# Kernel optimization log

Measured on AMD Instinct MI355X. Metric: run time of the kernel, lower is better.

## Reference

```python
import jax, jax.numpy as jnp
import numpy as np

N = 86016      # 1024 graphs x 84 nodes
E = 4194304    # directed edges
H = 32         # hidden size
B = 1024       # graphs per batch
NPG = 84       # nodes per graph (hardcoded in original forward)
DEPTH = 4      # args.depth
NEG_SLOPE = 0.2


def setup_inputs() -> dict:
    key = jax.random.key(0)
    ks = jax.random.split(key, 12)
    s = 0.1
    return {
        "x": jax.random.normal(ks[0], (N, 1), jnp.float32),
        "edge_index": jax.random.randint(ks[1], (2, E), 0, N, jnp.int64 if jax.config.jax_enable_x64 else jnp.int32),
        "edge_attr": jax.random.normal(ks[2], (E, 2), jnp.float32),
        "W0": jax.random.normal(ks[3], (1, H), jnp.float32) * s,
        "Ws": jax.random.normal(ks[4], (DEPTH - 1, H, H), jnp.float32) * s,
        "att_src": jax.random.normal(ks[5], (DEPTH, H), jnp.float32) * s,
        "att_dst": jax.random.normal(ks[6], (DEPTH, H), jnp.float32) * s,
        "We": jax.random.normal(ks[7], (DEPTH, 2, H), jnp.float32) * s,
        "att_edge": jax.random.normal(ks[8], (DEPTH, H), jnp.float32) * s,
        "bias": jnp.zeros((DEPTH, H), jnp.float32),
        "lin_w": jax.random.normal(ks[9], (H, 1), jnp.float32) * s,
        "lin_b": jnp.zeros((1,), jnp.float32),
    }


def _gat_layer(h_in, src, dst, ea, W, a_s, a_d, We_l, a_e, b):
    """PyG GATConv, heads=1, edge_dim set, self-loops already appended.
    src/dst: [E+N] indices; ea: [E+N, edge_dim] edge attrs (with mean-filled loops)."""
    h = h_in @ W                                  # [N, H]
    alpha_src = h @ a_s                           # [N]
    alpha_dst = h @ a_d                           # [N]
    # fold lin_edge + att_edge: (ea @ We) @ a_e == ea @ (We @ a_e) -> avoids [E,H]
    alpha_edge = ea @ (We_l @ a_e)                # [E+N]
    logits = alpha_src[src] + alpha_dst[dst] + alpha_edge
    logits = jnp.where(logits >= 0, logits, NEG_SLOPE * logits)  # leaky_relu(0.2)
    # segment softmax over destination nodes (every node has a self-loop -> nonempty)
    m = jax.ops.segment_max(logits, dst, num_segments=N)
    w = jnp.exp(logits - m[dst])
    denom = jax.ops.segment_sum(w, dst, num_segments=N)
    alpha = w / denom[dst]                        # [E+N]
    out = jax.ops.segment_sum(alpha[:, None] * h[src], dst, num_segments=N)
    return out + b


def reference(x, edge_index, edge_attr, W0, Ws, att_src, att_dst, We, att_edge, bias, lin_w, lin_b):
    src0, dst0 = edge_index[0], edge_index[1]
    # add_self_loops with fill_value='mean': per-dst mean of incoming edge attrs
    deg = jax.ops.segment_sum(jnp.ones((E,), x.dtype), dst0, num_segments=N)
    ea_loop = jax.ops.segment_sum(edge_attr, dst0, num_segments=N) / jnp.maximum(deg, 1.0)[:, None]
    loops = jnp.arange(N, dtype=src0.dtype)
    src = jnp.concatenate([src0, loops])
    dst = jnp.concatenate([dst0, loops])
    ea = jnp.concatenate([edge_attr, ea_loop], axis=0)

    # layer 0 (+ relu; dropout is identity in eval)
    h = _gat_layer(x, src, dst, ea, W0, att_src[0], att_dst[0], We[0], att_edge[0], bias[0])
    h = jax.nn.relu(h)
    # middle layers
    for i in range(1, DEPTH - 1):
        h = _gat_layer(h, src, dst, ea, Ws[i - 1], att_src[i], att_dst[i], We[i], att_edge[i], bias[i])
        h = jax.nn.relu(h)
    # last layer: no relu/dropout
    h = _gat_layer(h, src, dst, ea, Ws[DEPTH - 2], att_src[DEPTH - 1], att_dst[DEPTH - 1],
                   We[DEPTH - 1], att_edge[DEPTH - 1], bias[DEPTH - 1])

    # global_add_pool over 84-node graphs, then linear + relu
    graph_ids = jnp.repeat(jnp.arange(B), NPG)    # [N]
    pooled = jax.ops.segment_sum(h, graph_ids, num_segments=B)  # [B, H]
    return jax.nn.relu(pooled @ lin_w + lin_b)    # [B, 1]
```

## Files before the change

### kernel.cpp

```cpp
#include <hip/hip_runtime.h>

#define N_NODES 86016
#define N_EDGES 4194304
#define HID 32
#define B_GR 1024
#define NPG 84
#define NEG 0.2f

#define NCH 512
#define CHE 8192
#define NB  512
#define NPB 168
#define SRCMASK 0x1FFFF

typedef float floatx2 __attribute__((ext_vector_type(2)));

constexpr size_t O_REC   = 0;
constexpr size_t O_CM    = O_REC  + (size_t)N_EDGES * 8;
constexpr size_t O_HT    = O_CM   + (size_t)NB * NCH * 4;
constexpr size_t O_HB    = O_HT   + (size_t)N_NODES * HID;
constexpr size_t O_AS    = O_HB   + (size_t)N_NODES * HID * 4;
constexpr size_t O_AD    = O_AS   + (size_t)N_NODES * 4;
constexpr size_t O_ROW   = O_AD   + (size_t)N_NODES * 4;
constexpr size_t O_BTOT  = O_ROW  + (size_t)(N_NODES + 1) * 4 + 12;
constexpr size_t O_BBASE = O_BTOT + (size_t)NB * 4;
constexpr size_t O_FOLD  = O_BBASE + (size_t)(NB + 1) * 4 + 12;

__device__ __forceinline__ unsigned short f2bf(float f) {
    unsigned u = __float_as_uint(f);
    u += 0x7FFFu + ((u >> 16) & 1u);
    return (unsigned short)(u >> 16);
}

__global__ __launch_bounds__(1024) void k_hist(const int* __restrict__ dst, int* __restrict__ cm) {
    __shared__ int cnt[NB];
    int t = threadIdx.x, c = blockIdx.x;
    if (t < NB) cnt[t] = 0;
    __syncthreads();
    int base = c * CHE;
#pragma unroll
    for (int k = 0; k < 8; ++k) {
        int d = dst[base + k * 1024 + t];
        atomicAdd(&cnt[(unsigned)d / NPB], 1);
    }
    __syncthreads();
    if (t < NB) cm[t * NCH + c] = cnt[t];
}

__global__ __launch_bounds__(512) void k_scanchunks(int* __restrict__ cm, int* __restrict__ btot) {
    __shared__ int sa[NCH], sb[NCH];
    int b = blockIdx.x, t = threadIdx.x;
    sa[t] = cm[b * NCH + t];
    __syncthreads();
    int* s = sa; int* d = sb;
    for (int off = 1; off < NCH; off <<= 1) {
        d[t] = s[t] + (t >= off ? s[t - off] : 0);
        __syncthreads();
        int* tmp = s; s = d; d = tmp;
    }
    cm[b * NCH + t] = t ? s[t - 1] : 0;
    if (t == 0) btot[b] = s[NCH - 1];
}

__global__ void k_scanbuckets(const int* __restrict__ btot, int* __restrict__ bbase,
                              int* __restrict__ row,
                              const float* __restrict__ We, const float* __restrict__ ae,
                              float* __restrict__ fold) {
    __shared__ int sa[NB], sb[NB];
    int t = threadIdx.x;
    if (t < 8) {
        int l = t >> 1, c = t & 1;
        float s = 0.f;
        for (int j = 0; j < 32; ++j) s += We[l * 64 + c * 32 + j] * ae[l * 32 + j];
        fold[t] = s;
    }
    sa[t] = btot[t];
    __syncthreads();
    int* s = sa; int* d = sb;
    for (int off = 1; off < NB; off <<= 1) {
        d[t] = s[t] + (t >= off ? s[t - off] : 0);
        __syncthreads();
        int* tmp = s; s = d; d = tmp;
    }
    bbase[t] = t ? s[t - 1] : 0;
    if (t == NB - 1) { bbase[NB] = s[NB - 1]; row[N_NODES] = s[NB - 1]; }
}

__global__ __launch_bounds__(1024) void k_place(const int* __restrict__ ei,
                                                const float2* __restrict__ ea,
                                                const int* __restrict__ cm,
                                                const int* __restrict__ bbase,
                                                int2* __restrict__ rec) {
    __shared__ int cnt[NB];
    __shared__ int base[NB];
    int t = threadIdx.x, c = blockIdx.x;
    if (t < NB) cnt[t] = 0;
    __syncthreads();
    int eb = c * CHE;
    int wd0[8], bin[8], rnk[8];
    unsigned pk[8];
#pragma unroll
    for (int k = 0; k < 8; ++k) {
        int e = eb + k * 1024 + t;
        int s = ei[e];
        int d = ei[N_EDGES + e];
        float2 a = ea[e];
        int b = (unsigned)d / NPB;
        int dn = d - b * NPB;
        wd0[k] = s | (dn << 17);
        pk[k] = ((unsigned)f2bf(a.y) << 16) | f2bf(a.x);
        bin[k] = b;
        rnk[k] = atomicAdd(&cnt[b], 1);
    }
    __syncthreads();
    if (t < NB) base[t] = bbase[t] + cm[t * NCH + c];
    __syncthreads();
#pragma unroll
    for (int k = 0; k < 8; ++k)
        rec[base[bin[k]] + rnk[k]] = make_int2(wd0[k], (int)pk[k]);
}

__global__ __launch_bounds__(1024) void k_sort(int2* __restrict__ rec,
                                               const int* __restrict__ bbase,
                                               int* __restrict__ row) {
    __shared__ int cnt[256], tmp[256], ebase[256];
    int b = blockIdx.x, t = threadIdx.x;
    int n0 = b * NPB;
    int beg = bbase[b], end = bbase[b + 1], m = end - beg;
    if (t < 256) cnt[t] = 0;
    __syncthreads();
    int2 rv[12];
    int dr[12];
    int cv = 0;
    for (int i = t; i < m; i += 1024) {
        int2 r = rec[beg + i];
        int dn = ((unsigned)r.x >> 17) & 0xFF;
        int rnk = atomicAdd(&cnt[dn], 1);
        if (cv < 12) { rv[cv] = r; dr[cv] = dn | (rnk << 8); }
        cv++;
    }
    __syncthreads();
    int* s = cnt; int* d = tmp;
    for (int off = 1; off < 256; off <<= 1) {
        int v = 0;
        if (t < 256) v = s[t] + (t >= off ? s[t - off] : 0);
        __syncthreads();
        if (t < 256) d[t] = v;
        __syncthreads();
        int* tp = s; s = d; d = tp;
    }
    if (t < 256) ebase[t] = t ? s[t - 1] : 0;
    __syncthreads();
    if (t < NPB) row[n0 + t] = beg + ebase[t];
    int ncv = cv < 12 ? cv : 12;
    for (int k = 0; k < ncv; ++k) {
        int dn = dr[k] & 0xFF;
        int rnk = dr[k] >> 8;
        rec[beg + ebase[dn] + rnk] = rv[k];
    }
}

__device__ __forceinline__ void store_fp8_pair(unsigned short* __restrict__ hout,
                                               int n, int j, float acc) {
    float p = __shfl_xor(acc, 1);
    if (!(j & 1)) {
        int pk = __builtin_amdgcn_cvt_pk_fp8_f32(acc, p, 0, false);
        hout[(n << 4) + (j >> 1)] = (unsigned short)pk;
    }
}

__global__ void k_transform0(const float* __restrict__ x, const float* __restrict__ W0,
                             const float* __restrict__ as_w, const float* __restrict__ ad_w,
                             unsigned short* __restrict__ hout, float* __restrict__ as_arr,
                             float* __restrict__ ad_arr) {
    int tid = blockIdx.x * 256 + threadIdx.x;
    int j = tid & 31;
    int n = tid >> 5;
    float acc = x[n] * W0[j];
    store_fp8_pair(hout, n, j, acc);
    float v1 = acc * as_w[j], v2 = acc * ad_w[j];
#pragma unroll
    for (int m = 16; m >= 1; m >>= 1) {
        v1 += __shfl_xor(v1, m);
        v2 += __shfl_xor(v2, m);
    }
    if (j == 0) { as_arr[n] = v1; ad_arr[n] = v2; }
}

__global__ void k_transform(const float* __restrict__ hin, const float* __restrict__ W,
                            const float* __restrict__ as_w, const float* __restrict__ ad_w,
                            unsigned short* __restrict__ hout, float* __restrict__ as_arr,
                            float* __restrict__ ad_arr) {
    __shared__ float Wl[1024];
    int t = threadIdx.x;
#pragma unroll
    for (int i = 0; i < 4; ++i) Wl[t + i * 256] = W[t + i * 256];
    __syncthreads();
    int tid = blockIdx.x * 256 + t;
    int j = tid & 31;
    int n = tid >> 5;
    float hv = hin[tid];
    float acc = 0.f;
#pragma unroll
    for (int k = 0; k < 32; ++k) acc += __shfl(hv, k, 32) * Wl[k * 32 + j];
    store_fp8_pair(hout, n, j, acc);
    float v1 = acc * as_w[j], v2 = acc * ad_w[j];
#pragma unroll
    for (int m = 16; m >= 1; m >>= 1) {
        v1 += __shfl_xor(v1, m);
        v2 += __shfl_xor(v2, m);
    }
    if (j == 0) { as_arr[n] = v1; ad_arr[n] = v2; }
}

__device__ __forceinline__ void acc4_fp8(float w, int word, float* acc) {
    floatx2 v01 = __builtin_amdgcn_cvt_pk_f32_fp8(word, false);
    floatx2 v23 = __builtin_amdgcn_cvt_pk_f32_fp8(word, true);
    acc[0] = fmaf(w, v01.x, acc[0]);
    acc[1] = fmaf(w, v01.y, acc[1]);
    acc[2] = fmaf(w, v23.x, acc[2]);
    acc[3] = fmaf(w, v23.y, acc[3]);
}

__device__ __forceinline__ void edge_body(int2 r, const int2* __restrict__ hv,
                                          const float* __restrict__ as_arr,
                                          float c_dst, float f0, float f1, int dl,
                                          float* acc, float& den, float& esum) {
    int s = r.x & SRCMASK;
    int2 h = hv[(s << 2) + dl];
    float a = as_arr[s];
    float ax = __uint_as_float((unsigned)r.y << 16);
    float ay = __uint_as_float((unsigned)r.y & 0xFFFF0000u);
    float ed = fmaf(ax, f0, ay * f1);
    float lg = a + c_dst + ed;
    lg = fmaxf(lg, NEG * lg);
    float w = __expf(lg);
    den += w;
    esum += ed;
    acc4_fp8(w, h.x, acc);
    acc4_fp8(w, h.y, acc + 4);
}

__global__ void k_gather(const unsigned short* __restrict__ hT, const int2* __restrict__ rec,
                         const int* __restrict__ row,
                         const float* __restrict__ as_arr, const float* __restrict__ ad_arr,
                         const float* __restrict__ fold, const float* __restrict__ bias,
                         float* __restrict__ out, int do_relu) {
    const int2* hv = (const int2*)hT;
    int lane = threadIdx.x & 63;
    int n = blockIdx.x * 4 + (threadIdx.x >> 6);
    int slot = lane >> 2;
    int dl = lane & 3;
    int beg = row[n], end = row[n + 1];
    float c_dst = ad_arr[n];
    float f0 = fold[0], f1 = fold[1];
    float acc[8] = {0.f, 0.f, 0.f, 0.f, 0.f, 0.f, 0.f, 0.f};
    float den = 0.f, esum = 0.f;
    int e = beg;
    for (; e + 32 <= end; e += 32) {
        int2 r0 = rec[e + slot];
        int2 r1 = rec[e + 16 + slot];
        edge_body(r0, hv, as_arr, c_dst, f0, f1, dl, acc, den, esum);
        edge_body(r1, hv, as_arr, c_dst, f0, f1, dl, acc, den, esum);
    }
    for (; e + 16 <= end; e += 16) {
        int2 r = rec[e + slot];
        edge_body(r, hv, as_arr, c_dst, f0, f1, dl, acc, den, esum);
    }
    {
        int ee = e + slot;
        if (ee < end)
            edge_body(rec[ee], hv, as_arr, c_dst, f0, f1, dl, acc, den, esum);
    }
#pragma unroll
    for (int m = 4; m <= 32; m <<= 1) {
#pragma unroll
        for (int k = 0; k < 8; ++k) acc[k] += __shfl_xor(acc[k], m);
        den += __shfl_xor(den, m);
        esum += __shfl_xor(esum, m);
    }
    int dg = end - beg;
    float el = esum / fmaxf((float)dg, 1.0f);
    float lg = as_arr[n] + c_dst + el;
    lg = fmaxf(lg, NEG * lg);
    float w = __expf(lg);
    den += w;
    int2 hs = hv[(n << 2) + dl];
    acc4_fp8(w, hs.x, acc);
    acc4_fp8(w, hs.y, acc + 4);
    float rden = 1.0f / den;
    float o[8];
#pragma unroll
    for (int k = 0; k < 8; ++k) {
        o[k] = acc[k] * rden + bias[8 * dl + k];
        if (do_relu) o[k] = fmaxf(o[k], 0.f);
    }
    if (slot == 0) {
        float4 v0 = {o[0], o[1], o[2], o[3]};
        float4 v1 = {o[4], o[5], o[6], o[7]};
        *(float4*)(out + (n << 5) + 8 * dl) = v0;
        *(float4*)(out + (n << 5) + 8 * dl + 4) = v1;
    }
}

__global__ void k_pool(const float* __restrict__ h, const float* __restrict__ lw,
                       const float* __restrict__ lb, float* __restrict__ out) {
    int lane = threadIdx.x & 63;
    int g = blockIdx.x * 4 + (threadIdx.x >> 6);
    int j = lane & 31;
    int half = lane >> 5;
    const float* base = h + (size_t)g * NPG * HID;
    float acc = 0.f;
    for (int i = half; i < NPG; i += 2) acc += base[i * HID + j];
    acc += __shfl_xor(acc, 32);
    float v = acc * lw[j];
#pragma unroll
    for (int m = 16; m >= 1; m >>= 1) v += __shfl_xor(v, m);
    if (lane == 0) out[g] = fmaxf(v + lb[0], 0.f);
}

extern "C" void kernel_launch(void* const* d_in, const int* in_sizes, int n_in,
                              void* d_out, int out_size, void* d_ws, size_t ws_size,
                              hipStream_t stream) {
    const float* x        = (const float*)d_in[0];
    const int*   ei       = (const int*)d_in[1];
    const float* eattr    = (const float*)d_in[2];
    const float* W0       = (const float*)d_in[3];
    const float* Ws       = (const float*)d_in[4];
    const float* att_src  = (const float*)d_in[5];
    const float* att_dst  = (const float*)d_in[6];
    const float* We       = (const float*)d_in[7];
    const float* att_edge = (const float*)d_in[8];
    const float* bias     = (const float*)d_in[9];
    const float* lin_w    = (const float*)d_in[10];
    const float* lin_b    = (const float*)d_in[11];
    float* out = (float*)d_out;

    char* w = (char*)d_ws;
    int2*           rec    = (int2*)(w + O_REC);
    int*            cm     = (int*)(w + O_CM);
    unsigned short* hT     = (unsigned short*)(w + O_HT);
    float*          hB     = (float*)(w + O_HB);
    float*          as_arr = (float*)(w + O_AS);
    float*          ad_arr = (float*)(w + O_AD);
    int*            row    = (int*)(w + O_ROW);
    int*            btot   = (int*)(w + O_BTOT);
    int*            bbase  = (int*)(w + O_BBASE);
    float*          fold   = (float*)(w + O_FOLD);

    k_hist<<<NCH, 1024, 0, stream>>>(ei + N_EDGES, cm);
    k_scanchunks<<<NB, 512, 0, stream>>>(cm, btot);
    k_scanbuckets<<<1, NB, 0, stream>>>(btot, bbase, row, We, att_edge, fold);
    k_place<<<NCH, 1024, 0, stream>>>(ei, (const float2*)eattr, cm, bbase, rec);
    k_sort<<<NB, 1024, 0, stream>>>(rec, bbase, row);

    k_transform0<<<N_NODES * HID / 256, 256, 0, stream>>>(x, W0, att_src, att_dst,
                                                          hT, as_arr, ad_arr);
    k_gather<<<N_NODES / 4, 256, 0, stream>>>(hT, rec, row, as_arr, ad_arr,
                                              fold, bias, hB, 1);
    for (int l = 1; l < 4; ++l) {
        k_transform<<<N_NODES * HID / 256, 256, 0, stream>>>(
            hB, Ws + (size_t)(l - 1) * HID * HID, att_src + l * HID, att_dst + l * HID,
            hT, as_arr, ad_arr);
        k_gather<<<N_NODES / 4, 256, 0, stream>>>(hT, rec, row, as_arr, ad_arr,
                                                  fold + 2 * l, bias + l * HID, hB,
                                                  (l < 3) ? 1 : 0);
    }

    k_pool<<<B_GR / 4, 256, 0, stream>>>(hB, lin_w, lin_b, out);
}
```

Before: 518.9 us.

## Compute edge weights once per lane and broadcast via shuffles in gather

The gather kernel now assigns one edge per lane for logit/exp computation over 64-edge chunks, then broadcasts source index and weight to feature lanes with shuffles, removing the 4x redundant record loads, attention loads and exponentials. Accumulation switches to packed two-wide FMA on float2 accumulators. The cost is extra shuffles and wasted work on inactive lanes in partial chunks, which is significant since average degree is below 64.

```diff
diff --git a/kernel.cpp b/kernel.cpp
--- a/kernel.cpp
+++ b/kernel.cpp
@@ -213,32 +213,11 @@
     if (j == 0) { as_arr[n] = v1; ad_arr[n] = v2; }
 }
 
-__device__ __forceinline__ void acc4_fp8(float w, int word, float* acc) {
+__device__ __forceinline__ void acc4_fp8_pk(floatx2 w2, int word, floatx2* acc) {
     floatx2 v01 = __builtin_amdgcn_cvt_pk_f32_fp8(word, false);
     floatx2 v23 = __builtin_amdgcn_cvt_pk_f32_fp8(word, true);
-    acc[0] = fmaf(w, v01.x, acc[0]);
-    acc[1] = fmaf(w, v01.y, acc[1]);
-    acc[2] = fmaf(w, v23.x, acc[2]);
-    acc[3] = fmaf(w, v23.y, acc[3]);
-}
-
-__device__ __forceinline__ void edge_body(int2 r, const int2* __restrict__ hv,
-                                          const float* __restrict__ as_arr,
-                                          float c_dst, float f0, float f1, int dl,
-                                          float* acc, float& den, float& esum) {
-    int s = r.x & SRCMASK;
-    int2 h = hv[(s << 2) + dl];
-    float a = as_arr[s];
-    float ax = __uint_as_float((unsigned)r.y << 16);
-    float ay = __uint_as_float((unsigned)r.y & 0xFFFF0000u);
-    float ed = fmaf(ax, f0, ay * f1);
-    float lg = a + c_dst + ed;
-    lg = fmaxf(lg, NEG * lg);
-    float w = __expf(lg);
-    den += w;
-    esum += ed;
-    acc4_fp8(w, h.x, acc);
-    acc4_fp8(w, h.y, acc + 4);
+    acc[0] = __builtin_elementwise_fma(w2, v01, acc[0]);
+    acc[1] = __builtin_elementwise_fma(w2, v23, acc[1]);
 }
 
 __global__ void k_gather(const unsigned short* __restrict__ hT, const int2* __restrict__ rec,
@@ -254,28 +233,44 @@
     int beg = row[n], end = row[n + 1];
     float c_dst = ad_arr[n];
     float f0 = fold[0], f1 = fold[1];
-    float acc[8] = {0.f, 0.f, 0.f, 0.f, 0.f, 0.f, 0.f, 0.f};
+    floatx2 acc2[4];
+    floatx2 zz = {0.f, 0.f};
+    acc2[0] = zz; acc2[1] = zz; acc2[2] = zz; acc2[3] = zz;
     float den = 0.f, esum = 0.f;
-    int e = beg;
-    for (; e + 32 <= end; e += 32) {
-        int2 r0 = rec[e + slot];
-        int2 r1 = rec[e + 16 + slot];
-        edge_body(r0, hv, as_arr, c_dst, f0, f1, dl, acc, den, esum);
-        edge_body(r1, hv, as_arr, c_dst, f0, f1, dl, acc, den, esum);
-    }
-    for (; e + 16 <= end; e += 16) {
-        int2 r = rec[e + slot];
-        edge_body(r, hv, as_arr, c_dst, f0, f1, dl, acc, den, esum);
-    }
-    {
-        int ee = e + slot;
-        if (ee < end)
-            edge_body(rec[ee], hv, as_arr, c_dst, f0, f1, dl, acc, den, esum);
-    }
+    for (int e = beg; e < end; e += 64) {
+        int ee = e + lane;
+        bool act = ee < end;
+        int2 r = rec[act ? ee : end - 1];
+        int s = r.x & SRCMASK;
+        float a = as_arr[s];
+        float ax = __uint_as_float((unsigned)r.y << 16);
+        float ay = __uint_as_float((unsigned)r.y & 0xFFFF0000u);
+        float ed = fmaf(ax, f0, ay * f1);
+        float lg = a + c_dst + ed;
+        lg = fmaxf(lg, NEG * lg);
+        float w = act ? __expf(lg) : 0.f;
+        den += w;
+        esum += act ? ed : 0.f;
+#pragma unroll
+        for (int p = 0; p < 4; ++p) {
+            int sl = p * 16 + slot;
+            int sp = __shfl(s, sl);
+            float wp = __shfl(w, sl);
+            int2 h = hv[(sp << 2) + dl];
+            floatx2 w2 = {wp, wp};
+            acc4_fp8_pk(w2, h.x, acc2);
+            acc4_fp8_pk(w2, h.y, acc2 + 2);
+        }
+    }
+    float* accf = (float*)acc2;
+    den += __shfl_xor(den, 1);
+    den += __shfl_xor(den, 2);
+    esum += __shfl_xor(esum, 1);
+    esum += __shfl_xor(esum, 2);
 #pragma unroll
     for (int m = 4; m <= 32; m <<= 1) {
 #pragma unroll
-        for (int k = 0; k < 8; ++k) acc[k] += __shfl_xor(acc[k], m);
+        for (int k = 0; k < 8; ++k) accf[k] += __shfl_xor(accf[k], m);
         den += __shfl_xor(den, m);
         esum += __shfl_xor(esum, m);
     }
@@ -286,13 +281,14 @@
     float w = __expf(lg);
     den += w;
     int2 hs = hv[(n << 2) + dl];
-    acc4_fp8(w, hs.x, acc);
-    acc4_fp8(w, hs.y, acc + 4);
+    floatx2 w2 = {w, w};
+    acc4_fp8_pk(w2, hs.x, acc2);
+    acc4_fp8_pk(w2, hs.y, acc2 + 2);
     float rden = 1.0f / den;
     float o[8];
 #pragma unroll
     for (int k = 0; k < 8; ++k) {
-        o[k] = acc[k] * rden + bias[8 * dl + k];
+        o[k] = accf[k] * rden + bias[8 * dl + k];
         if (do_relu) o[k] = fmaxf(o[k], 0.f);
     }
     if (slot == 0) {
```

New measurement: 505.6 us. -2.6%, faster.
